# Optimization experiments

Measured on AMD Instinct MI355X. Metric: run time of the kernel, lower is better.

## Reference

```python
import jax, jax.numpy as jnp
import numpy as np

BST_DEPTH = 10                      # tree depth
NB_SPLIT = 2 ** BST_DEPTH - 1       # 1023 internal (split) nodes
NB_NODES = 2 ** (BST_DEPTH + 1) - 1 # 2047 total nodes
N = 32768                           # batch size
IN_SIZE = 255                       # raw feature dim (dim = IN_SIZE + 1 after bias concat)


def setup_inputs() -> dict:
    key = jax.random.key(0)
    k1, k2, k3 = jax.random.split(key, 3)
    dim = IN_SIZE + 1
    X = jax.random.normal(k1, (N, IN_SIZE), dtype=jnp.float32)
    # A ~ U[0,1) as in torch.rand
    A = jax.random.uniform(k2, (NB_SPLIT, dim), dtype=jnp.float32)
    W = jax.random.normal(k3, (1, dim + NB_NODES), dtype=jnp.float32) * 0.02
    b = jnp.zeros((1,), dtype=jnp.float32)
    return {"X": X, "A": A, "W": W, "b": b}


def _latent_tree_z(x, A):
    """Equivalent of LatentTree._compute_q + clamp, unpruned.

    The torch code initializes q=1, scatters min(1, +/-XA) into children, then
    propagates parent mins down for `depth` iterations. The fixed point it
    reaches is exactly q_t = min(q_parent(t), sign_t * XA[:, parent(t)]) computed
    level by level (root q = 1), which is what we build here.
    """
    XA = x @ A.T  # [N, nb_split]
    n = x.shape[0]
    q_levels = [jnp.ones((n, 1), x.dtype)]  # root
    for l in range(1, BST_DEPTH + 1):
        t = np.arange(2 ** l - 1, 2 ** (l + 1) - 1)      # node ids at level l
        parent = (t - 1) // 2                            # split-node ids
        sign = np.where(t % 2 == 1, 1.0, -1.0).astype(np.float32)  # left:+, right:-
        e = XA[:, parent] * sign[None, :]                # edge values [N, 2^l]
        prev_off = 2 ** (l - 1) - 1
        q_parent = q_levels[-1][:, parent - prev_off]    # gather parent q
        q_levels.append(jnp.minimum(q_parent, e))
    q = jnp.concatenate(q_levels, axis=1)  # [N, nb_nodes]
    return jnp.clip(q, 0.0, 1.0)


def reference(X, A, W, b):
    # append bias column of ones
    x = jnp.concatenate([X, jnp.ones((X.shape[0], 1), X.dtype)], axis=1)
    z = _latent_tree_z(x, A)                 # [N, nb_nodes]
    xz = jnp.concatenate([x, z], axis=1)     # [N, dim + nb_nodes]
    return jax.nn.sigmoid(xz @ W.T + b)      # [N, 1]
```

## Files before the change

### kernel.cpp

```cpp
#include <hip/hip_runtime.h>

typedef __attribute__((ext_vector_type(8))) short    bf16x8;
typedef __attribute__((ext_vector_type(4))) float    f32x4;
typedef __attribute__((ext_vector_type(4))) float    float4_t;
typedef __attribute__((ext_vector_type(4))) unsigned u32x4;

constexpr int NSAMP    = 32768;
constexpr int INSZ     = 255;
constexpr int DIM      = 256;
constexpr int NSPLIT   = 1023;
constexpr int NCOL     = 1024;
constexpr int BM       = 64;
constexpr int NTHREADS = 512;
constexpr int NMT      = 4;
constexpr int NPASS    = 8;

constexpr int XA_OFF    = 32768;
constexpr int LDS_BYTES = XA_OFF + NCOL * 128;
constexpr size_t WS_NEED = (size_t)NCOL * DIM * 2;

extern __shared__ char smem[];

__device__ __forceinline__ short f2bf(float f) {
  unsigned x = __builtin_bit_cast(unsigned, f);
  x += 0x7fffu + ((x >> 16) & 1u);
  return (short)(x >> 16);
}
__device__ __forceinline__ float bfraw(unsigned hw16) {
  return __builtin_bit_cast(float, hw16 << 16);
}
__device__ __forceinline__ unsigned cvt_pk(float lo, float hi) {
  unsigned r;
  asm("v_cvt_pk_bf16_f32 %0, %1, %2" : "=v"(r) : "v"(lo), "v"(hi));
  return r;
}
__device__ __forceinline__ float clamp01(float v) {
  return fminf(fmaxf(v, 0.f), 1.f);
}

__device__ __forceinline__ int xat_sw(int node) {
  return ((node & 15) << 3) | ((node & 1) << 2);
}
__device__ __forceinline__ float xat_read(const char* __restrict__ xat, int t, int lane2) {
  unsigned hw = *(const unsigned short*)(xat + t * 128 + (lane2 ^ xat_sw(t)));
  return bfraw(hw);
}

__global__ void prep_frag(const float* __restrict__ A, const float* __restrict__ W,
                          u32x4* __restrict__ wsf)
{
  int t    = blockIdx.x * 512 + threadIdx.x;
  int lane = t & 63;
  int ks   = (t >> 6) & 7;
  int ct   = t >> 9;
  int col  = ct * 16 + (lane & 15);
  int k0   = ks * 32 + ((lane >> 4) << 3);
  const float* src = (col < NSPLIT) ? (A + col * DIM + k0) : (W + k0);
  float4_t a0 = *(const float4_t*)src;
  float4_t a1 = *(const float4_t*)(src + 4);
  u32x4 p;
  p[0] = cvt_pk(a0[0], a0[1]);
  p[1] = cvt_pk(a0[2], a0[3]);
  p[2] = cvt_pk(a1[0], a1[1]);
  p[3] = cvt_pk(a1[2], a1[3]);
  wsf[t] = p;
}

template<bool USE_WS>
__device__ __forceinline__ void load_bfr(int ct, bf16x8* dst, int lane,
                                         const u32x4* __restrict__ wsf,
                                         const float* __restrict__ A,
                                         const float* __restrict__ W)
{
  if constexpr (USE_WS) {
    const u32x4* fp = wsf + ct * 512 + lane;
#pragma unroll
    for (int ks = 0; ks < 8; ++ks)
      dst[ks] = __builtin_bit_cast(bf16x8, fp[ks * 64]);
  } else {
    int col = ct * 16 + (lane & 15);
    int k0  = (lane >> 4) << 3;
    const float* ap = (col < NSPLIT) ? (A + col * DIM) : W;
#pragma unroll
    for (int ks = 0; ks < 8; ++ks) {
      float4_t a0 = *(const float4_t*)(ap + ks * 32 + k0);
      float4_t a1 = *(const float4_t*)(ap + ks * 32 + k0 + 4);
      unsigned q0 = ((unsigned)(unsigned short)f2bf(a0[0])) | (((unsigned)(unsigned short)f2bf(a0[1])) << 16);
      unsigned q1 = ((unsigned)(unsigned short)f2bf(a0[2])) | (((unsigned)(unsigned short)f2bf(a0[3])) << 16);
      unsigned q2 = ((unsigned)(unsigned short)f2bf(a1[0])) | (((unsigned)(unsigned short)f2bf(a1[1])) << 16);
      unsigned q3 = ((unsigned)(unsigned short)f2bf(a1[2])) | (((unsigned)(unsigned short)f2bf(a1[3])) << 16);
      u32x4 p = {q0, q1, q2, q3};
      dst[ks] = __builtin_bit_cast(bf16x8, p);
    }
  }
}

template<int D>
__device__ __forceinline__ void dfs(int t, float q, float& acc,
                                    const char* __restrict__ xat, int lane2,
                                    const float* __restrict__ Wz)
{
  if (__ballot(q > 0.f) == 0ull) return;
  float xa = xat_read(xat, t, lane2);
  float qL = fminf(q, xa);
  float qR = fminf(q, -xa);
  acc += clamp01(qL) * Wz[2 * t + 1] + clamp01(qR) * Wz[2 * t + 2];
  if constexpr (D > 1) {
    dfs<D - 1>(2 * t + 1, qL, acc, xat, lane2, Wz);
    dfs<D - 1>(2 * t + 2, qR, acc, xat, lane2, Wz);
  }
}

template<bool USE_WS>
__global__ __launch_bounds__(NTHREADS) __attribute__((amdgpu_waves_per_eu(2, 2)))
void lt_main(const float* __restrict__ X, const float* __restrict__ A,
             const float* __restrict__ W, const float* __restrict__ Bv,
             const u32x4* __restrict__ wsf, float* __restrict__ Out)
{
  const int tid  = threadIdx.x;
  const int lane = tid & 63;
  const int wave = tid >> 6;
  const int m0   = blockIdx.x * BM;

  bf16x8 b0[8], b1[8];
  load_bfr<USE_WS>(wave, b0, lane, wsf, A, W);

  {
    const float4_t* Xt = (const float4_t*)(X + (size_t)m0 * INSZ);
#pragma unroll
    for (int i = 0; i < 8; ++i) {
      int idx = tid + i * NTHREADS;
      if (idx < 4080) {
        float4_t v = Xt[idx];
#pragma unroll
        for (int e = 0; e < 4; ++e) {
          int g   = idx * 4 + e;
          int row = g / 255;
          int col = g - row * 255;
          *(short*)(smem + (((row << 9) + (col << 1)) ^ ((row & 7) << 4))) = f2bf(v[e]);
        }
      }
    }
    if (tid < BM)
      *(short*)(smem + (((tid << 9) + (255 << 1)) ^ ((tid & 7) << 4))) = (short)0x3f80;
  }
  __syncthreads();

  bf16x8 xf[NMT][8];
#pragma unroll
  for (int mt = 0; mt < NMT; ++mt) {
    int row = mt * 16 + (lane & 15);
#pragma unroll
    for (int ks = 0; ks < 8; ++ks) {
      int kk = ks * 32 + ((lane >> 4) << 3);
      xf[mt][ks] = *(const bf16x8*)(smem + (((row << 9) + (kk << 1)) ^ ((row & 7) << 4)));
    }
  }

  char* xat = smem + XA_OFF;

#pragma unroll
  for (int p = 0; p < NPASS; ++p) {
    bf16x8* cur = (p & 1) ? b1 : b0;
    bf16x8* nxt = (p & 1) ? b0 : b1;
    if (p < NPASS - 1)
      load_bfr<USE_WS>((p + 1) * 8 + wave, nxt, lane, wsf, A, W);

    f32x4 acc[NMT];
#pragma unroll
    for (int mt = 0; mt < NMT; ++mt) acc[mt] = f32x4{0.f, 0.f, 0.f, 0.f};
#pragma unroll
    for (int ks = 0; ks < 8; ++ks) {
#pragma unroll
      for (int mt = 0; mt < NMT; ++mt)
        acc[mt] = __builtin_amdgcn_mfma_f32_16x16x32_bf16(xf[mt][ks], cur[ks], acc[mt], 0, 0, 0);
    }

    int node = (p * 8 + wave) * 16 + (lane & 15);
    int sw   = xat_sw(node);
    char* xrow = xat + node * 128;
#pragma unroll
    for (int mt = 0; mt < NMT; ++mt) {
#pragma unroll
      for (int h = 0; h < 2; ++h) {
        int s0 = mt * 16 + ((lane >> 4) << 2) + h * 2;
        unsigned lo = (unsigned short)f2bf(acc[mt][2 * h]);
        unsigned hi = (unsigned short)f2bf(acc[mt][2 * h + 1]);
        *(unsigned*)(xrow + ((s0 * 2) ^ sw)) = lo | (hi << 16);
      }
    }
  }
  __syncthreads();

  const float* Wz    = W + DIM;
  const int    lane2 = lane << 1;

  int s3 = 7 + wave;
  int a2 = (s3 - 1) >> 1;
  int a1 = (a2 - 1) >> 1;
  float q = 1.f;
  {
    float x0 = xat_read(xat, 0,  lane2); q = fminf(q, (a1 & 1) ? x0 : -x0);
    float x1 = xat_read(xat, a1, lane2); q = fminf(q, (a2 & 1) ? x1 : -x1);
    float x2 = xat_read(xat, a2, lane2); q = fminf(q, (s3 & 1) ? x2 : -x2);
  }
  float acc = 0.f;
  dfs<7>(s3, q, acc, xat, lane2, Wz);
  if (wave == 0)
    dfs<3>(0, 1.f, acc, xat, lane2, Wz);

  float* part = (float*)smem;
  part[(wave << 6) + lane] = acc;
  __syncthreads();

  if (tid < BM) {
    float sum = 0.f;
#pragma unroll
    for (int w = 0; w < 8; ++w) sum += part[(w << 6) + tid];
    float xw = xat_read(xat, 1023, tid << 1);
    float v  = sum + xw + Bv[0] + Wz[0];
    Out[m0 + tid] = 1.f / (1.f + __expf(-v));
  }
}

extern "C" void kernel_launch(void* const* d_in, const int* in_sizes, int n_in,
                              void* d_out, int out_size, void* d_ws, size_t ws_size,
                              hipStream_t stream) {
  (void)in_sizes; (void)n_in; (void)out_size;
  const float* X  = (const float*)d_in[0];
  const float* A  = (const float*)d_in[1];
  const float* W  = (const float*)d_in[2];
  const float* Bv = (const float*)d_in[3];
  float* Out = (float*)d_out;

  const bool use_ws = (d_ws != nullptr) && (ws_size >= WS_NEED);
  if (use_ws) {
    prep_frag<<<64, 512, 0, stream>>>(A, W, (u32x4*)d_ws);
    hipFuncSetAttribute(reinterpret_cast<const void*>(lt_main<true>),
                        hipFuncAttributeMaxDynamicSharedMemorySize, LDS_BYTES);
    lt_main<true><<<NSAMP / BM, NTHREADS, LDS_BYTES, stream>>>(
        X, A, W, Bv, (const u32x4*)d_ws, Out);
  } else {
    hipFuncSetAttribute(reinterpret_cast<const void*>(lt_main<false>),
                        hipFuncAttributeMaxDynamicSharedMemorySize, LDS_BYTES);
    lt_main<false><<<NSAMP / BM, NTHREADS, LDS_BYTES, stream>>>(
        X, A, W, Bv, nullptr, Out);
  }
}
```

Before: 39.39 us.

## Assign each wave its own subtree columns to drop the post-GEMM barrier

```diff
diff --git a/kernel.cpp b/kernel.cpp
--- a/kernel.cpp
+++ b/kernel.cpp
@@ -9,15 +9,15 @@
 constexpr int INSZ     = 255;
 constexpr int DIM      = 256;
 constexpr int NSPLIT   = 1023;
-constexpr int NCOL     = 1024;
 constexpr int BM       = 64;
 constexpr int NTHREADS = 512;
 constexpr int NMT      = 4;
-constexpr int NPASS    = 8;
+constexpr int NPASS    = 9;
+constexpr int NTILES   = 72;
 
 constexpr int XA_OFF    = 32768;
-constexpr int LDS_BYTES = XA_OFF + NCOL * 128;
-constexpr size_t WS_NEED = (size_t)NCOL * DIM * 2;
+constexpr int LDS_BYTES = XA_OFF + 1024 * 128;
+constexpr size_t WS_NEED = (size_t)NTILES * 512 * 16;
 
 extern __shared__ char smem[];
 
@@ -38,6 +38,19 @@
   return fminf(fmaxf(v, 0.f), 1.f);
 }
 
+__device__ __forceinline__ int cmap(int w, int t, int i) {
+  if (t == 0) { int j = i & 7; return (j == 7) ? NSPLIT : j; }
+  if (t == 1) {
+    if (i == 0 || i == 15) return 7 + w;
+    if (i <= 2)  return 14 + 2 * w + i;
+    if (i <= 6)  return 28 + 4 * w + i;
+    return 56 + 8 * w + i;
+  }
+  if (t == 2) return 127 + 16 * w + i;
+  if (t <= 4) return 255 + 32 * w + (t - 3) * 16 + i;
+  return 511 + 64 * w + (t - 5) * 16 + i;
+}
+
 __device__ __forceinline__ int xat_sw(int node) {
   return ((node & 15) << 3) | ((node & 1) << 2);
 }
@@ -49,11 +62,11 @@
 __global__ void prep_frag(const float* __restrict__ A, const float* __restrict__ W,
                           u32x4* __restrict__ wsf)
 {
-  int t    = blockIdx.x * 512 + threadIdx.x;
-  int lane = t & 63;
-  int ks   = (t >> 6) & 7;
-  int ct   = t >> 9;
-  int col  = ct * 16 + (lane & 15);
+  int w    = blockIdx.x / NPASS;
+  int t    = blockIdx.x % NPASS;
+  int lane = threadIdx.x & 63;
+  int ks   = (threadIdx.x >> 6) & 7;
+  int col  = cmap(w, t, lane & 15);
   int k0   = ks * 32 + ((lane >> 4) << 3);
   const float* src = (col < NSPLIT) ? (A + col * DIM + k0) : (W + k0);
   float4_t a0 = *(const float4_t*)src;
@@ -63,7 +76,7 @@
   p[1] = cvt_pk(a0[2], a0[3]);
   p[2] = cvt_pk(a1[0], a1[1]);
   p[3] = cvt_pk(a1[2], a1[3]);
-  wsf[t] = p;
+  wsf[blockIdx.x * 512 + threadIdx.x] = p;
 }
 
 template<bool USE_WS>
@@ -78,7 +91,7 @@
     for (int ks = 0; ks < 8; ++ks)
       dst[ks] = __builtin_bit_cast(bf16x8, fp[ks * 64]);
   } else {
-    int col = ct * 16 + (lane & 15);
+    int col = cmap(ct / NPASS, ct % NPASS, lane & 15);
     int k0  = (lane >> 4) << 3;
     const float* ap = (col < NSPLIT) ? (A + col * DIM) : W;
 #pragma unroll
@@ -123,7 +136,7 @@
   const int m0   = blockIdx.x * BM;
 
   bf16x8 b0[8], b1[8];
-  load_bfr<USE_WS>(wave, b0, lane, wsf, A, W);
+  load_bfr<USE_WS>(wave * NPASS, b0, lane, wsf, A, W);
 
   {
     const float4_t* Xt = (const float4_t*)(X + (size_t)m0 * INSZ);
@@ -156,6 +169,7 @@
       xf[mt][ks] = *(const bf16x8*)(smem + (((row << 9) + (kk << 1)) ^ ((row & 7) << 4)));
     }
   }
+  __syncthreads();
 
   char* xat = smem + XA_OFF;
 
@@ -164,7 +178,7 @@
     bf16x8* cur = (p & 1) ? b1 : b0;
     bf16x8* nxt = (p & 1) ? b0 : b1;
     if (p < NPASS - 1)
-      load_bfr<USE_WS>((p + 1) * 8 + wave, nxt, lane, wsf, A, W);
+      load_bfr<USE_WS>(wave * NPASS + p + 1, nxt, lane, wsf, A, W);
 
     f32x4 acc[NMT];
 #pragma unroll
@@ -176,7 +190,7 @@
         acc[mt] = __builtin_amdgcn_mfma_f32_16x16x32_bf16(xf[mt][ks], cur[ks], acc[mt], 0, 0, 0);
     }
 
-    int node = (p * 8 + wave) * 16 + (lane & 15);
+    int node = cmap(wave, p, lane & 15);
     int sw   = xat_sw(node);
     char* xrow = xat + node * 128;
 #pragma unroll
@@ -190,7 +204,6 @@
       }
     }
   }
-  __syncthreads();
 
   const float* Wz    = W + DIM;
   const int    lane2 = lane << 1;
@@ -217,7 +230,7 @@
     float sum = 0.f;
 #pragma unroll
     for (int w = 0; w < 8; ++w) sum += part[(w << 6) + tid];
-    float xw = xat_read(xat, 1023, tid << 1);
+    float xw = xat_read(xat, NSPLIT, tid << 1);
     float v  = sum + xw + Bv[0] + Wz[0];
     Out[m0 + tid] = 1.f / (1.f + __expf(-v));
   }
@@ -235,7 +248,7 @@
 
   const bool use_ws = (d_ws != nullptr) && (ws_size >= WS_NEED);
   if (use_ws) {
-    prep_frag<<<64, 512, 0, stream>>>(A, W, (u32x4*)d_ws);
+    prep_frag<<<NTILES, 512, 0, stream>>>(A, W, (u32x4*)d_ws);
     hipFuncSetAttribute(reinterpret_cast<const void*>(lt_main<true>),
                         hipFuncAttributeMaxDynamicSharedMemorySize, LDS_BYTES);
     lt_main<true><<<NSAMP / BM, NTHREADS, LDS_BYTES, stream>>>(
```

Result: slower. 40.95 us (+4.0%).

## Process two 64-row halves per block with X prefetch overlapping tree walk

Applied to the files above, without the earlier changes.

```diff
diff --git a/kernel.cpp b/kernel.cpp
--- a/kernel.cpp
+++ b/kernel.cpp
@@ -10,7 +10,8 @@
 constexpr int DIM      = 256;
 constexpr int NSPLIT   = 1023;
 constexpr int NCOL     = 1024;
-constexpr int BM       = 64;
+constexpr int BM       = 128;
+constexpr int HALF     = 64;
 constexpr int NTHREADS = 512;
 constexpr int NMT      = 4;
 constexpr int NPASS    = 8;
@@ -95,12 +96,74 @@
   }
 }
 
+__device__ __forceinline__ void xwrite_elem(int g, float v) {
+  int row = g / 255;
+  int col = g - row * 255;
+  *(short*)(smem + (((row << 9) + (col << 1)) ^ ((row & 7) << 4))) = f2bf(v);
+}
+__device__ __forceinline__ void xwrite_bias(int tid) {
+  if (tid < HALF)
+    *(short*)(smem + (((tid << 9) + (255 << 1)) ^ ((tid & 7) << 4))) = (short)0x3f80;
+}
+__device__ __forceinline__ void preload_xf(bf16x8 (&xf)[NMT][8], int lane) {
+#pragma unroll
+  for (int mt = 0; mt < NMT; ++mt) {
+    int row = mt * 16 + (lane & 15);
+#pragma unroll
+    for (int ks = 0; ks < 8; ++ks) {
+      int kk = ks * 32 + ((lane >> 4) << 3);
+      xf[mt][ks] = *(const bf16x8*)(smem + (((row << 9) + (kk << 1)) ^ ((row & 7) << 4)));
+    }
+  }
+}
+
+template<bool USE_WS>
+__device__ __forceinline__ void phase1(bf16x8 (&xf)[NMT][8], bf16x8* b0, bf16x8* b1,
+                                       int wave, int lane,
+                                       const u32x4* __restrict__ wsf,
+                                       const float* __restrict__ A,
+                                       const float* __restrict__ W, char* xat)
+{
+#pragma unroll
+  for (int p = 0; p < NPASS; ++p) {
+    bf16x8* cur = (p & 1) ? b1 : b0;
+    bf16x8* nxt = (p & 1) ? b0 : b1;
+    if (p < NPASS - 1)
+      load_bfr<USE_WS>((p + 1) * 8 + wave, nxt, lane, wsf, A, W);
+
+    f32x4 acc[NMT];
+#pragma unroll
+    for (int mt = 0; mt < NMT; ++mt) acc[mt] = f32x4{0.f, 0.f, 0.f, 0.f};
+#pragma unroll
+    for (int ks = 0; ks < 8; ++ks) {
+#pragma unroll
+      for (int mt = 0; mt < NMT; ++mt)
+        acc[mt] = __builtin_amdgcn_mfma_f32_16x16x32_bf16(xf[mt][ks], cur[ks], acc[mt], 0, 0, 0);
+    }
+    int node = (p * 8 + wave) * 16 + (lane & 15);
+    int sw   = xat_sw(node);
+    char* xrow = xat + node * 128;
+#pragma unroll
+    for (int mt = 0; mt < NMT; ++mt) {
+#pragma unroll
+      for (int h = 0; h < 2; ++h) {
+        int s0 = mt * 16 + ((lane >> 4) << 2) + h * 2;
+        unsigned lo = (unsigned short)f2bf(acc[mt][2 * h]);
+        unsigned hi = (unsigned short)f2bf(acc[mt][2 * h + 1]);
+        *(unsigned*)(xrow + ((s0 * 2) ^ sw)) = lo | (hi << 16);
+      }
+    }
+  }
+}
+
 template<int D>
 __device__ __forceinline__ void dfs(int t, float q, float& acc,
                                     const char* __restrict__ xat, int lane2,
                                     const float* __restrict__ Wz)
 {
-  if (__ballot(q > 0.f) == 0ull) return;
+  if constexpr (D > 1) {
+    if (__ballot(q > 0.f) == 0ull) return;
+  }
   float xa = xat_read(xat, t, lane2);
   float qL = fminf(q, xa);
   float qR = fminf(q, -xa);
@@ -111,6 +174,27 @@
   }
 }
 
+__device__ __forceinline__ float walk(const char* __restrict__ xat, int wave, int lane2,
+                                      const float* __restrict__ Wz)
+{
+  int s3 = 7 + wave;
+  int a2 = (s3 - 1) >> 1;
+  int a1 = (a2 - 1) >> 1;
+  float q = 1.f;
+  float x0 = xat_read(xat, 0,  lane2); q = fminf(q, (a1 & 1) ? x0 : -x0);
+  float x1 = xat_read(xat, a1, lane2); q = fminf(q, (a2 & 1) ? x1 : -x1);
+  float x2 = xat_read(xat, a2, lane2); q = fminf(q, (s3 & 1) ? x2 : -x2);
+  float acc = 0.f;
+  dfs<7>(s3, q, acc, xat, lane2, Wz);
+  if (wave == 0)
+    dfs<3>(0, 1.f, acc, xat, lane2, Wz);
+  return acc;
+}
+
+__device__ __forceinline__ float* part_base(char* xat, int w) {
+  return (float*)(xat + (size_t)(520 + 64 * w) * 128);
+}
+
 template<bool USE_WS>
 __global__ __launch_bounds__(NTHREADS) __attribute__((amdgpu_waves_per_eu(2, 2)))
 void lt_main(const float* __restrict__ X, const float* __restrict__ A,
@@ -121,6 +205,9 @@
   const int lane = tid & 63;
   const int wave = tid >> 6;
   const int m0   = blockIdx.x * BM;
+  char* xat = smem + XA_OFF;
+  const float* Wz = W + DIM;
+  const float bias = Bv[0] + Wz[0];
 
   bf16x8 b0[8], b1[8];
   load_bfr<USE_WS>(wave, b0, lane, wsf, A, W);
@@ -133,93 +220,73 @@
       if (idx < 4080) {
         float4_t v = Xt[idx];
 #pragma unroll
-        for (int e = 0; e < 4; ++e) {
-          int g   = idx * 4 + e;
-          int row = g / 255;
-          int col = g - row * 255;
-          *(short*)(smem + (((row << 9) + (col << 1)) ^ ((row & 7) << 4))) = f2bf(v[e]);
-        }
+        for (int e = 0; e < 4; ++e) xwrite_elem(idx * 4 + e, v[e]);
       }
     }
-    if (tid < BM)
-      *(short*)(smem + (((tid << 9) + (255 << 1)) ^ ((tid & 7) << 4))) = (short)0x3f80;
+    xwrite_bias(tid);
   }
   __syncthreads();
 
   bf16x8 xf[NMT][8];
-#pragma unroll
-  for (int mt = 0; mt < NMT; ++mt) {
-    int row = mt * 16 + (lane & 15);
-#pragma unroll
-    for (int ks = 0; ks < 8; ++ks) {
-      int kk = ks * 32 + ((lane >> 4) << 3);
-      xf[mt][ks] = *(const bf16x8*)(smem + (((row << 9) + (kk << 1)) ^ ((row & 7) << 4)));
-    }
-  }
-
-  char* xat = smem + XA_OFF;
-
-#pragma unroll
-  for (int p = 0; p < NPASS; ++p) {
-    bf16x8* cur = (p & 1) ? b1 : b0;
-    bf16x8* nxt = (p & 1) ? b0 : b1;
-    if (p < NPASS - 1)
-      load_bfr<USE_WS>((p + 1) * 8 + wave, nxt, lane, wsf, A, W);
-
-    f32x4 acc[NMT];
-#pragma unroll
-    for (int mt = 0; mt < NMT; ++mt) acc[mt] = f32x4{0.f, 0.f, 0.f, 0.f};
-#pragma unroll
-    for (int ks = 0; ks < 8; ++ks) {
-#pragma unroll
-      for (int mt = 0; mt < NMT; ++mt)
-        acc[mt] = __builtin_amdgcn_mfma_f32_16x16x32_bf16(xf[mt][ks], cur[ks], acc[mt], 0, 0, 0);
-    }
-
-    int node = (p * 8 + wave) * 16 + (lane & 15);
-    int sw   = xat_sw(node);
-    char* xrow = xat + node * 128;
-#pragma unroll
-    for (int mt = 0; mt < NMT; ++mt) {
-#pragma unroll
-      for (int h = 0; h < 2; ++h) {
-        int s0 = mt * 16 + ((lane >> 4) << 2) + h * 2;
-        unsigned lo = (unsigned short)f2bf(acc[mt][2 * h]);
-        unsigned hi = (unsigned short)f2bf(acc[mt][2 * h + 1]);
-        *(unsigned*)(xrow + ((s0 * 2) ^ sw)) = lo | (hi << 16);
+  preload_xf(xf, lane);
+
+  phase1<USE_WS>(xf, b0, b1, wave, lane, wsf, A, W, xat);
+  __syncthreads();
+
+  float4_t xr[8];
+  {
+    const float4_t* Xt1 = (const float4_t*)(X + (size_t)(m0 + HALF) * INSZ);
+#pragma unroll
+    for (int i = 0; i < 8; ++i) {
+      int idx = tid + i * NTHREADS;
+      if (idx < 4080) xr[i] = Xt1[idx];
+    }
+  }
+  load_bfr<USE_WS>(wave, b0, lane, wsf, A, W);
+
+  {
+    float acc = walk(xat, wave, lane << 1, Wz);
+    part_base(xat, wave)[lane] = acc;
+  }
+  __syncthreads();
+
+  if (tid < HALF) {
+    float sum = 0.f;
+#pragma unroll
+    for (int w = 0; w < 8; ++w) sum += part_base(xat, w)[tid];
+    float xw = xat_read(xat, 1023, tid << 1);
+    Out[m0 + tid] = 1.f / (1.f + __expf(-(sum + xw + bias)));
+  }
+  {
+#pragma unroll
+    for (int i = 0; i < 8; ++i) {
+      int idx = tid + i * NTHREADS;
+      if (idx < 4080) {
+        float4_t v = xr[i];
+#pragma unroll
+        for (int e = 0; e < 4; ++e) xwrite_elem(idx * 4 + e, v[e]);
       }
     }
-  }
-  __syncthreads();
-
-  const float* Wz    = W + DIM;
-  const int    lane2 = lane << 1;
-
-  int s3 = 7 + wave;
-  int a2 = (s3 - 1) >> 1;
-  int a1 = (a2 - 1) >> 1;
-  float q = 1.f;
-  {
-    float x0 = xat_read(xat, 0,  lane2); q = fminf(q, (a1 & 1) ? x0 : -x0);
-    float x1 = xat_read(xat, a1, lane2); q = fminf(q, (a2 & 1) ? x1 : -x1);
-    float x2 = xat_read(xat, a2, lane2); q = fminf(q, (s3 & 1) ? x2 : -x2);
-  }
-  float acc = 0.f;
-  dfs<7>(s3, q, acc, xat, lane2, Wz);
-  if (wave == 0)
-    dfs<3>(0, 1.f, acc, xat, lane2, Wz);
-
-  float* part = (float*)smem;
-  part[(wave << 6) + lane] = acc;
-  __syncthreads();
-
-  if (tid < BM) {
+    xwrite_bias(tid);
+  }
+  __syncthreads();
+
+  preload_xf(xf, lane);
+  phase1<USE_WS>(xf, b0, b1, wave, lane, wsf, A, W, xat);
+  __syncthreads();
+
+  {
+    float acc = walk(xat, wave, lane << 1, Wz);
+    part_base(xat, wave)[lane] = acc;
+  }
+  __syncthreads();
+
+  if (tid < HALF) {
     float sum = 0.f;
 #pragma unroll
-    for (int w = 0; w < 8; ++w) sum += part[(w << 6) + tid];
+    for (int w = 0; w < 8; ++w) sum += part_base(xat, w)[tid];
     float xw = xat_read(xat, 1023, tid << 1);
-    float v  = sum + xw + Bv[0] + Wz[0];
-    Out[m0 + tid] = 1.f / (1.f + __expf(-v));
+    Out[m0 + HALF + tid] = 1.f / (1.f + __expf(-(sum + xw + bias)));
   }
 }
 
```

Measured after the change: 81.25 us. +106.3%, slower.
